# Kernel optimization log

Measured on AMD Instinct MI355X. Metric: run time of the kernel, lower is better.

Reference implementation:

```python
import jax, jax.numpy as jnp
import numpy as np

B, SQ, SK, D = 8, 2048, 768, 768  # SK must equal D for layer_combine concat to typecheck


def setup_inputs() -> dict:
    key = jax.random.key(0)
    ks = jax.random.split(key, 13)
    s = 0.02
    return {
        "query": jax.random.normal(ks[0], (B, SQ, D), jnp.float32),
        "key_matrix": jax.random.normal(ks[1], (B, SK, D), jnp.float32),
        "value_matrix": jax.random.normal(ks[2], (B, SK, D), jnp.float32),
        "prev_layer": jax.random.normal(ks[3], (SK, D), jnp.float32) * s,
        "attention_mask": jax.random.randint(ks[4], (B, 1, SK), 0, 2, jnp.int32),
        "Wq": jax.random.normal(ks[5], (D, D), jnp.float32) * s,
        "bq": jax.random.normal(ks[6], (D,), jnp.float32) * s,
        "Wk": jax.random.normal(ks[7], (D, D), jnp.float32) * s,
        "bk": jax.random.normal(ks[8], (D,), jnp.float32) * s,
        "Wv": jax.random.normal(ks[9], (D, D), jnp.float32) * s,
        "bv": jax.random.normal(ks[10], (D,), jnp.float32) * s,
        "Wc": jax.random.normal(ks[11], (D, 2 * D), jnp.float32) * s,
        "bc": jax.random.normal(ks[12], (D,), jnp.float32) * s,
    }


def reference(query, key_matrix, value_matrix, prev_layer, attention_mask,
              Wq, bq, Wk, bk, Wv, bv, Wc, bc):
    # Linear projections (torch Linear: x @ W.T + b)
    Q = query @ Wq.T + bq                      # [B, SQ, D]
    K = key_matrix @ Wk.T + bk                 # [B, SK, D]
    V = value_matrix @ Wv.T + bv               # computed but unused when prev_layer given (faithful)
    scale = 1.0 / np.sqrt(D).astype(np.float32)
    scores = jnp.einsum('bqd,bkd->bqk', Q, K) * scale  # [B, SQ, SK]
    scores = jnp.where(attention_mask == 0, jnp.float32(-1e9), scores)
    # prev-layer integration: matmul + concat + linear combine
    layer_attn = scores @ prev_layer           # [B, SQ, D]
    combined = jnp.concatenate([scores, layer_attn], axis=-1)  # [B, SQ, 2D]
    out = combined @ Wc.T + bc                 # [B, SQ, D]
    return out
```

## Files before the change

### kernel.cpp

```cpp
#include <hip/hip_runtime.h>
#include <hip/hip_bf16.h>


typedef __attribute__((ext_vector_type(8))) short short8;
typedef __attribute__((ext_vector_type(4))) float f32x4;

#define SCALE 0.03608439182435161f

__device__ inline unsigned short f2bf(float x) {
  unsigned int u = __builtin_bit_cast(unsigned int, x);
  u = (u + 0x7fffu + ((u >> 16) & 1u)) >> 16;
  return (unsigned short)u;
}
__device__ inline float bf2f(unsigned short h) {
  return __builtin_bit_cast(float, ((unsigned int)h) << 16);
}

__global__ void k_cvt8(const float* __restrict__ s, unsigned short* __restrict__ d, int n8) {
  int i = blockIdx.x * 256 + threadIdx.x;
  if (i >= n8) return;
  const float4* s4 = reinterpret_cast<const float4*>(s);
  float4 v0 = s4[2 * i], v1 = s4[2 * i + 1];
  ushort4* d4 = reinterpret_cast<ushort4*>(d);
  d4[2 * i]     = make_ushort4(f2bf(v0.x), f2bf(v0.y), f2bf(v0.z), f2bf(v0.w));
  d4[2 * i + 1] = make_ushort4(f2bf(v1.x), f2bf(v1.y), f2bf(v1.z), f2bf(v1.w));
}

__global__ void k_prep(const float* __restrict__ prev, const float* __restrict__ Wc,
                       unsigned short* __restrict__ prev_bf,
                       unsigned short* __restrict__ Wc2_bf) {
  int g = blockIdx.x;
  int region = g / 576;
  int idx = (g - region * 576) * 256 + threadIdx.x;
  float4 v;
  unsigned short* dst;
  if (region == 0) { v = reinterpret_cast<const float4*>(prev)[idx]; dst = prev_bf; }
  else {
    int r = idx / 192, c4 = (idx - r * 192) * 4;
    v = *reinterpret_cast<const float4*>(Wc + (long long)r * 1536 + 768 + c4);
    dst = Wc2_bf;
  }
  reinterpret_cast<ushort4*>(dst)[idx] = make_ushort4(f2bf(v.x), f2bf(v.y), f2bf(v.z), f2bf(v.w));
}

__global__ void k_tcvt(const float* __restrict__ Wq, const float* __restrict__ Wk,
                       const float* __restrict__ key, const int* __restrict__ mask,
                       unsigned short* __restrict__ WqT, unsigned short* __restrict__ WkT,
                       unsigned short* __restrict__ keyzT) {
  __shared__ float t[64][65];
  int z = blockIdx.z;
  const float* src;
  unsigned short* dst;
  const int* mb = nullptr;
  if (z == 0) { src = Wq; dst = WqT; }
  else if (z == 1) { src = Wk; dst = WkT; }
  else {
    int b = z - 2;
    src = key + (long long)b * 589824;
    dst = keyzT + (long long)b * 589824;
    mb = mask + b * 768;
  }
  int bx = blockIdx.x * 64, by = blockIdx.y * 64;
  int tx = threadIdx.x & 63, ty = threadIdx.x >> 6;
  #pragma unroll
  for (int i = 0; i < 64; i += 4) {
    float v = src[(long long)(by + ty + i) * 768 + bx + tx];
    if (mb) v = mb[by + ty + i] ? v : 0.0f;
    t[ty + i][tx] = v;
  }
  __syncthreads();
  #pragma unroll
  for (int i = 0; i < 64; i += 4)
    dst[(long long)(bx + ty + i) * 768 + by + tx] = f2bf(t[tx][ty + i]);
}

__global__ void k_sums(const unsigned short* __restrict__ WqT,
                       const unsigned short* __restrict__ WkT,
                       const float* __restrict__ bk, const float* __restrict__ bq,
                       const float* __restrict__ Mt, const int* __restrict__ mask,
                       float* __restrict__ u, float* __restrict__ w3,
                       float* __restrict__ s1, float* __restrict__ sm0) {
  int gw = blockIdx.x * 4 + (threadIdx.x >> 6);
  int lane = threadIdx.x & 63;
  if (gw < 1536) {
    const unsigned short* wrow = (gw < 768) ? (WqT + (long long)gw * 768)
                                            : (WkT + (long long)(gw - 768) * 768);
    const float* vec = (gw < 768) ? bk : bq;
    float s = 0.f;
    for (int j = lane; j < 768; j += 64) s += bf2f(wrow[j]) * vec[j];
    #pragma unroll
    for (int off = 32; off > 0; off >>= 1) s += __shfl_down(s, off, 64);
    if (lane == 0) { if (gw < 768) u[gw] = s; else w3[gw - 768] = s; }
  } else {
    int g2 = gw - 1536;
    int b = g2 / 768, d2 = g2 - b * 768;
    if (b >= 8) return;
    const int* mb = mask + b * 768;
    const float* mrow = Mt + (long long)d2 * 768;
    float a1 = 0.f, a0 = 0.f;
    for (int k = lane; k < 768; k += 64) {
      float v = mrow[k];
      if (mb[k]) a1 += v; else a0 += v;
    }
    #pragma unroll
    for (int off = 32; off > 0; off >>= 1) {
      a1 += __shfl_down(a1, off, 64);
      a0 += __shfl_down(a0, off, 64);
    }
    if (lane == 0) { s1[g2] = a1; sm0[g2] = a0; }
  }
}

__global__ void k_row(const unsigned short* __restrict__ Tt, const float* __restrict__ w3,
                      const float* __restrict__ s1, const float* __restrict__ sm0,
                      const float* __restrict__ bq, const float* __restrict__ bk,
                      const float* __restrict__ bc, float* __restrict__ row) {
  int gw = blockIdx.x * 4 + (threadIdx.x >> 6);
  int lane = threadIdx.x & 63;
  int b = gw / 768, d2 = gw - b * 768;
  if (b >= 8) return;
  const unsigned short* trow = Tt + ((long long)b * 768 + d2) * 768;
  float st = 0.f, sbb = 0.f;
  for (int j = lane; j < 768; j += 64) {
    st += bf2f(trow[j]) * w3[j];
    sbb += bq[j] * bk[j];
  }
  #pragma unroll
  for (int off = 32; off > 0; off >>= 1) {
    st += __shfl_down(st, off, 64);
    sbb += __shfl_down(sbb, off, 64);
  }
  if (lane == 0)
    row[gw] = bc[d2] - 1e9f * sm0[gw] + SCALE * (st + sbb * s1[gw]);
}

template <int MODE>
__global__ __launch_bounds__(256) void gemm_nt(
    const unsigned short* __restrict__ A, long long aStr, int lda,
    const unsigned short* __restrict__ B, long long bStr, int ldb,
    float* __restrict__ Cf, unsigned short* __restrict__ Cbf,
    long long cStr, int ldc,
    const float* __restrict__ aux, const float* __restrict__ aux2)
{
  constexpr int BM = 64, BN = 64, BK = 64;
  __shared__ __align__(16) char As[BM * BK * 2];
  __shared__ __align__(16) char Bs[BN * BK * 2];

  const int gx = gridDim.x, gy = gridDim.y;
  const int nwg = gx * gy * (int)gridDim.z;
  int lin = blockIdx.x + gx * (blockIdx.y + gy * blockIdx.z);
  int qq = nwg >> 3, rr = nwg & 7, xcd = lin & 7, loc = lin >> 3;
  int swz = (xcd < rr ? xcd * (qq + 1) : rr * (qq + 1) + (xcd - rr) * qq) + loc;
  int bz = swz / (gx * gy);
  int rem = swz - bz * gx * gy;
  int by = rem / gx, bx = rem - by * gx;

  const int b = bz;
  const unsigned short* Ab = A + (long long)b * aStr;
  const unsigned short* Bb = B + (long long)b * bStr;
  const int m0 = by * BM, n0 = bx * BN;

  const int tid = threadIdx.x;
  const int w = tid >> 6, lane = tid & 63;
  const int wr = w >> 1, wc = w & 1;
  const int fr = lane & 15, fq = lane >> 4;

  f32x4 acc[2][2] = {};

  for (int kt = 0; kt < 768; kt += BK) {
    __syncthreads();
    #pragma unroll
    for (int t = 0; t < 2; ++t) {
      int g = t * 256 + tid;
      int row = g >> 3, s = g & 7;
      int sg = (s - row) & 7;
      const unsigned short* ga = Ab + (long long)(m0 + row) * lda + kt + sg * 8;
      __builtin_amdgcn_global_load_lds(
          (const __attribute__((address_space(1))) void*)ga,
          (__attribute__((address_space(3))) void*)(As + g * 16), 16, 0, 0);
    }
    #pragma unroll
    for (int t = 0; t < 2; ++t) {
      int g = t * 256 + tid;
      int row = g >> 3, s = g & 7;
      int sg = (s - row) & 7;
      const unsigned short* gb = Bb + (long long)(n0 + row) * ldb + kt + sg * 8;
      __builtin_amdgcn_global_load_lds(
          (const __attribute__((address_space(1))) void*)gb,
          (__attribute__((address_space(3))) void*)(Bs + g * 16), 16, 0, 0);
    }
    __syncthreads();

    #pragma unroll
    for (int kk = 0; kk < 2; ++kk) {
      short8 af[2], bfr[2];
      #pragma unroll
      for (int i = 0; i < 2; ++i) {
        int r = wr * 32 + i * 16 + fr;
        int sgi = ((kk * 4 + fq) + r) & 7;
        af[i] = *reinterpret_cast<const short8*>(As + r * 128 + sgi * 16);
      }
      #pragma unroll
      for (int j = 0; j < 2; ++j) {
        int r = wc * 32 + j * 16 + fr;
        int sgj = ((kk * 4 + fq) + r) & 7;
        bfr[j] = *reinterpret_cast<const short8*>(Bs + r * 128 + sgj * 16);
      }
      #pragma unroll
      for (int i = 0; i < 2; ++i)
        #pragma unroll
        for (int j = 0; j < 2; ++j)
          acc[i][j] = __builtin_amdgcn_mfma_f32_16x16x32_bf16(af[i], bfr[j], acc[i][j], 0, 0, 0);
    }
  }

  #pragma unroll
  for (int i = 0; i < 2; ++i)
    #pragma unroll
    for (int j = 0; j < 2; ++j)
      #pragma unroll
      for (int r = 0; r < 4; ++r) {
        int row = m0 + wr * 32 + i * 16 + fq * 4 + r;
        int col = n0 + wc * 32 + j * 16 + fr;
        float v = acc[i][j][r];
        if constexpr (MODE == 0) {
          v += aux[(long long)row * 1536 + col];
          Cf[(long long)row * 768 + col] = v;
          Cbf[(long long)row * 768 + col] = f2bf(v);
        } else if constexpr (MODE == 2) {
          Cbf[(long long)b * cStr + (long long)row * ldc + col] = f2bf(v);
        } else {
          v += aux[b * 768 + row] * aux2[col];
          Cbf[(long long)b * cStr + (long long)row * ldc + col] = f2bf(v);
        }
      }
}

__global__ __launch_bounds__(512, 1) void g5_pipe(
    const unsigned short* __restrict__ A,
    const unsigned short* __restrict__ B,
    float* __restrict__ C, const float* __restrict__ rowv)
{
  __shared__ __align__(16) char As[3][256 * 128];
  __shared__ __align__(16) char Bs[2][192 * 128];

  int lin = blockIdx.x + 4 * (blockIdx.y + 8 * blockIdx.z);
  int swz = (lin & 7) * 32 + (lin >> 3);
  int bz = swz >> 5;
  int rem = swz & 31;
  int by = rem >> 2, bx = rem & 3;

  const int b = bz;
  const int m0 = by * 256, n0 = bx * 192;
  const unsigned short* Ab = A + (long long)b * 1572864;
  const unsigned short* Bb = B + (long long)b * 589824;

  const int tid = threadIdx.x;
  const int w = tid >> 6, lane = tid & 63;
  const int wr = w >> 2, wn = w & 3;
  const int fr = lane & 15, fq = lane >> 4;

  f32x4 acc[8][3] = {};

  auto stageA = [&](int buf, int kt, int s0, int ns) {
    for (int s = s0; s < s0 + ns; ++s) {
      int g = s * 512 + tid;
      int row = g >> 3, slot = g & 7;
      int sg = (slot - row) & 7;
      const unsigned short* ga = Ab + (long long)(m0 + row) * 768 + kt + sg * 8;
      __builtin_amdgcn_global_load_lds(
          (const __attribute__((address_space(1))) void*)ga,
          (__attribute__((address_space(3))) void*)(&As[buf][0] + g * 16), 16, 0, 0);
    }
  };
  auto stageB = [&](int buf, int kt, int s0, int ns) {
    for (int s = s0; s < s0 + ns; ++s) {
      int g = s * 512 + tid;
      int row = g >> 3, slot = g & 7;
      int sg = (slot - row) & 7;
      const unsigned short* gb = Bb + (long long)(n0 + row) * 768 + kt + sg * 8;
      __builtin_amdgcn_global_load_lds(
          (const __attribute__((address_space(1))) void*)gb,
          (__attribute__((address_space(3))) void*)(&Bs[buf][0] + g * 16), 16, 0, 0);
    }
  };

  stageA(0, 0, 0, 4);
  stageB(0, 0, 0, 3);
  stageA(1, 64, 0, 4);
  asm volatile("s_waitcnt vmcnt(4)" ::: "memory");
  __builtin_amdgcn_s_barrier();

  for (int t = 0; t < 12; ++t) {
    const char* as = &As[t % 3][0];
    const char* bs = &Bs[t & 1][0];
    const int ktn1 = (t + 1) * 64, ktn2 = (t + 2) * 64;
    short8 a0[4], a1[4], bb[3];

    #pragma unroll
    for (int i = 0; i < 4; ++i) {
      int r = wr * 128 + i * 16 + fr;
      a0[i] = *reinterpret_cast<const short8*>(as + r * 128 + (((fq) + r) & 7) * 16);
    }
    #pragma unroll
    for (int j = 0; j < 3; ++j) {
      int r = wn * 48 + j * 16 + fr;
      bb[j] = *reinterpret_cast<const short8*>(bs + r * 128 + (((fq) + r) & 7) * 16);
    }
    if (t < 11) stageB((t + 1) & 1, ktn1, 0, 2);
    __builtin_amdgcn_s_barrier();
    __builtin_amdgcn_s_setprio(1);
    #pragma unroll
    for (int i = 0; i < 4; ++i)
      #pragma unroll
      for (int j = 0; j < 3; ++j)
        acc[i][j] = __builtin_amdgcn_mfma_f32_16x16x32_bf16(a0[i], bb[j], acc[i][j], 0, 0, 0);
    __builtin_amdgcn_s_setprio(0);
    __builtin_amdgcn_s_barrier();

    #pragma unroll
    for (int i = 0; i < 4; ++i) {
      int r = wr * 128 + (4 + i) * 16 + fr;
      a1[i] = *reinterpret_cast<const short8*>(as + r * 128 + (((fq) + r) & 7) * 16);
    }
    if (t < 11) stageB((t + 1) & 1, ktn1, 2, 1);
    if (t < 10) stageA((t + 2) % 3, ktn2, 0, 2);
    __builtin_amdgcn_s_barrier();
    __builtin_amdgcn_s_setprio(1);
    #pragma unroll
    for (int i = 0; i < 4; ++i)
      #pragma unroll
      for (int j = 0; j < 3; ++j)
        acc[4 + i][j] = __builtin_amdgcn_mfma_f32_16x16x32_bf16(a1[i], bb[j], acc[4 + i][j], 0, 0, 0);
    __builtin_amdgcn_s_setprio(0);
    __builtin_amdgcn_s_barrier();

    #pragma unroll
    for (int i = 0; i < 4; ++i) {
      int r = wr * 128 + i * 16 + fr;
      a0[i] = *reinterpret_cast<const short8*>(as + r * 128 + (((4 + fq) + r) & 7) * 16);
    }
    #pragma unroll
    for (int j = 0; j < 3; ++j) {
      int r = wn * 48 + j * 16 + fr;
      bb[j] = *reinterpret_cast<const short8*>(bs + r * 128 + (((4 + fq) + r) & 7) * 16);
    }
    if (t < 10) stageA((t + 2) % 3, ktn2, 2, 2);
    __builtin_amdgcn_s_barrier();
    __builtin_amdgcn_s_setprio(1);
    #pragma unroll
    for (int i = 0; i < 4; ++i)
      #pragma unroll
      for (int j = 0; j < 3; ++j)
        acc[i][j] = __builtin_amdgcn_mfma_f32_16x16x32_bf16(a0[i], bb[j], acc[i][j], 0, 0, 0);
    __builtin_amdgcn_s_setprio(0);
    __builtin_amdgcn_s_barrier();

    #pragma unroll
    for (int i = 0; i < 4; ++i) {
      int r = wr * 128 + (4 + i) * 16 + fr;
      a1[i] = *reinterpret_cast<const short8*>(as + r * 128 + (((4 + fq) + r) & 7) * 16);
    }
    __builtin_amdgcn_s_barrier();
    __builtin_amdgcn_s_setprio(1);
    #pragma unroll
    for (int i = 0; i < 4; ++i)
      #pragma unroll
      for (int j = 0; j < 3; ++j)
        acc[4 + i][j] = __builtin_amdgcn_mfma_f32_16x16x32_bf16(a1[i], bb[j], acc[4 + i][j], 0, 0, 0);
    __builtin_amdgcn_s_setprio(0);

    if (t < 10)       asm volatile("s_waitcnt vmcnt(4)" ::: "memory");
    else if (t == 10) asm volatile("s_waitcnt vmcnt(0)" ::: "memory");
    __builtin_amdgcn_s_barrier();
  }

  const long long ob = (long long)b * 1572864;
  #pragma unroll
  for (int i = 0; i < 8; ++i)
    #pragma unroll
    for (int j = 0; j < 3; ++j)
      #pragma unroll
      for (int r = 0; r < 4; ++r) {
        int row = m0 + wr * 128 + i * 16 + fq * 4 + r;
        int col = n0 + wn * 48 + j * 16 + fr;
        C[ob + (long long)row * 768 + col] = acc[i][j][r] * SCALE + rowv[b * 768 + col];
      }
}

extern "C" void kernel_launch(void* const* d_in, const int* in_sizes, int n_in,
                              void* d_out, int out_size, void* d_ws, size_t ws_size,
                              hipStream_t stream)
{
  const float* query = (const float*)d_in[0];
  const float* key   = (const float*)d_in[1];
  const float* prev  = (const float*)d_in[3];
  const int*   mask  = (const int*)d_in[4];
  const float* Wq    = (const float*)d_in[5];
  const float* bq    = (const float*)d_in[6];
  const float* Wk    = (const float*)d_in[7];
  const float* bk    = (const float*)d_in[8];
  const float* Wc    = (const float*)d_in[11];
  const float* bc    = (const float*)d_in[12];
  float* out = (float*)d_out;

  char* p = (char*)d_ws;
  size_t off = 0;
  auto alloc = [&](size_t bytes) {
    char* r = p + off;
    off += (bytes + 255) & ~(size_t)255;
    return r;
  };
  unsigned short* query_bf = (unsigned short*)alloc(12582912ull * 2);
  unsigned short* keyzT_bf = (unsigned short*)alloc(4718592ull * 2);
  unsigned short* WqT_bf   = (unsigned short*)alloc(589824ull * 2);
  unsigned short* WkT_bf   = (unsigned short*)alloc(589824ull * 2);
  unsigned short* prev_bf  = (unsigned short*)alloc(589824ull * 2);
  unsigned short* Wc2_bf   = (unsigned short*)alloc(589824ull * 2);
  float*          Mt_f     = (float*)alloc(589824ull * 4);
  unsigned short* Mt_bf    = (unsigned short*)alloc(589824ull * 2);
  unsigned short* W2_bf    = (unsigned short*)alloc(589824ull * 2);
  unsigned short* Tt_bf    = (unsigned short*)alloc(4718592ull * 2);
  unsigned short* Pt_bf    = (unsigned short*)alloc(4718592ull * 2);
  float*          s1f      = (float*)alloc(6144ull * 4);
  float*          sm0f     = (float*)alloc(6144ull * 4);
  float*          uv       = (float*)alloc(768ull * 4);
  float*          w3v      = (float*)alloc(768ull * 4);
  float*          rowv     = (float*)alloc(6144ull * 4);
  (void)ws_size; (void)in_sizes; (void)n_in; (void)out_size;

  k_cvt8<<<dim3(6144), dim3(256), 0, stream>>>(query, query_bf, 1572864);
  k_tcvt<<<dim3(12, 12, 10), dim3(256), 0, stream>>>(Wq, Wk, key, mask,
                                                     WqT_bf, WkT_bf, keyzT_bf);
  k_prep<<<dim3(1152), dim3(256), 0, stream>>>(prev, Wc, prev_bf, Wc2_bf);

  gemm_nt<0><<<dim3(12, 12, 1), dim3(256), 0, stream>>>(
      Wc2_bf, 0ll, 768, prev_bf, 0ll, 768, Mt_f, Mt_bf, 0ll, 768,
      Wc, (const float*)nullptr);
  gemm_nt<2><<<dim3(12, 12, 1), dim3(256), 0, stream>>>(
      WqT_bf, 0ll, 768, WkT_bf, 0ll, 768, (float*)nullptr, W2_bf, 0ll, 768,
      (const float*)nullptr, (const float*)nullptr);
  k_sums<<<dim3(1920), dim3(256), 0, stream>>>(WqT_bf, WkT_bf, bk, bq, Mt_f, mask,
                                               uv, w3v, s1f, sm0f);
  gemm_nt<2><<<dim3(12, 12, 8), dim3(256), 0, stream>>>(
      Mt_bf, 0ll, 768, keyzT_bf, 589824ll, 768, (float*)nullptr, Tt_bf,
      589824ll, 768, (const float*)nullptr, (const float*)nullptr);
  gemm_nt<5><<<dim3(12, 12, 8), dim3(256), 0, stream>>>(
      Tt_bf, 589824ll, 768, W2_bf, 0ll, 768, (float*)nullptr, Pt_bf,
      589824ll, 768, s1f, uv);
  k_row<<<dim3(1536), dim3(256), 0, stream>>>(Tt_bf, w3v, s1f, sm0f, bq, bk, bc, rowv);
  g5_pipe<<<dim3(4, 8, 8), dim3(512), 0, stream>>>(query_bf, Pt_bf, out, rowv);
}
```

Measured before the change: 115.4 us.

## Merge two weight GEMMs into one launch and simplify g5 pipeline schedule

Two independent 768x768 weight GEMMs (Wc2·prev and WqT·WkT) now run as one launch with a z-dimension of 2, saving a kernel launch and letting both fill the GPU together. The main g5_pipe loop drops its hand-interleaved four-phase schedule, which used split stage loads and many intra-iteration barriers. It now issues all prefetches for the next tiles at the top of each iteration and then runs two k-substeps, each loading all 8 A fragments and 3 B fragments before its MFMAs. This removes barrier overhead but loses fine-grained interleaving of loads with compute and raises register pressure with 8 A fragments live.

```diff
diff --git a/kernel.cpp b/kernel.cpp
--- a/kernel.cpp
+++ b/kernel.cpp
@@ -134,40 +134,26 @@
     row[gw] = bc[d2] - 1e9f * sm0[gw] + SCALE * (st + sbb * s1[gw]);
 }
 
-template <int MODE>
-__global__ __launch_bounds__(256) void gemm_nt(
-    const unsigned short* __restrict__ A, long long aStr, int lda,
-    const unsigned short* __restrict__ B, long long bStr, int ldb,
-    float* __restrict__ Cf, unsigned short* __restrict__ Cbf,
-    long long cStr, int ldc,
-    const float* __restrict__ aux, const float* __restrict__ aux2)
-{
-  constexpr int BM = 64, BN = 64, BK = 64;
-  __shared__ __align__(16) char As[BM * BK * 2];
-  __shared__ __align__(16) char Bs[BN * BK * 2];
-
+__device__ inline void xcd_swz(int& bx, int& by, int& bz) {
   const int gx = gridDim.x, gy = gridDim.y;
   const int nwg = gx * gy * (int)gridDim.z;
   int lin = blockIdx.x + gx * (blockIdx.y + gy * blockIdx.z);
   int qq = nwg >> 3, rr = nwg & 7, xcd = lin & 7, loc = lin >> 3;
   int swz = (xcd < rr ? xcd * (qq + 1) : rr * (qq + 1) + (xcd - rr) * qq) + loc;
-  int bz = swz / (gx * gy);
+  bz = swz / (gx * gy);
   int rem = swz - bz * gx * gy;
-  int by = rem / gx, bx = rem - by * gx;
-
-  const int b = bz;
-  const unsigned short* Ab = A + (long long)b * aStr;
-  const unsigned short* Bb = B + (long long)b * bStr;
-  const int m0 = by * BM, n0 = bx * BN;
-
-  const int tid = threadIdx.x;
+  by = rem / gx;
+  bx = rem - by * gx;
+}
+
+__device__ inline void nt64_core(const unsigned short* Ab, int lda,
+                                 const unsigned short* Bb, int ldb,
+                                 int m0, int n0, int tid, f32x4 (&acc)[2][2],
+                                 char* As, char* Bs) {
   const int w = tid >> 6, lane = tid & 63;
   const int wr = w >> 1, wc = w & 1;
   const int fr = lane & 15, fq = lane >> 4;
-
-  f32x4 acc[2][2] = {};
-
-  for (int kt = 0; kt < 768; kt += BK) {
+  for (int kt = 0; kt < 768; kt += 64) {
     __syncthreads();
     #pragma unroll
     for (int t = 0; t < 2; ++t) {
@@ -190,21 +176,18 @@
           (__attribute__((address_space(3))) void*)(Bs + g * 16), 16, 0, 0);
     }
     __syncthreads();
-
     #pragma unroll
     for (int kk = 0; kk < 2; ++kk) {
       short8 af[2], bfr[2];
       #pragma unroll
       for (int i = 0; i < 2; ++i) {
         int r = wr * 32 + i * 16 + fr;
-        int sgi = ((kk * 4 + fq) + r) & 7;
-        af[i] = *reinterpret_cast<const short8*>(As + r * 128 + sgi * 16);
+        af[i] = *reinterpret_cast<const short8*>(As + r * 128 + (((kk * 4 + fq) + r) & 7) * 16);
       }
       #pragma unroll
       for (int j = 0; j < 2; ++j) {
         int r = wc * 32 + j * 16 + fr;
-        int sgj = ((kk * 4 + fq) + r) & 7;
-        bfr[j] = *reinterpret_cast<const short8*>(Bs + r * 128 + sgj * 16);
+        bfr[j] = *reinterpret_cast<const short8*>(Bs + r * 128 + (((kk * 4 + fq) + r) & 7) * 16);
       }
       #pragma unroll
       for (int i = 0; i < 2; ++i)
@@ -213,7 +196,28 @@
           acc[i][j] = __builtin_amdgcn_mfma_f32_16x16x32_bf16(af[i], bfr[j], acc[i][j], 0, 0, 0);
     }
   }
-
+}
+
+__global__ __launch_bounds__(256) void gemm_g1w2(
+    const unsigned short* __restrict__ Wc2_bf, const unsigned short* __restrict__ prev_bf,
+    const unsigned short* __restrict__ WqT_bf, const unsigned short* __restrict__ WkT_bf,
+    const float* __restrict__ Wc, float* __restrict__ Mt_f,
+    unsigned short* __restrict__ Mt_bf, unsigned short* __restrict__ W2_bf)
+{
+  __shared__ __align__(16) char As[64 * 128];
+  __shared__ __align__(16) char Bs[64 * 128];
+  int bx, by, bz;
+  xcd_swz(bx, by, bz);
+  const int m0 = by * 64, n0 = bx * 64;
+  const unsigned short* A = bz ? WqT_bf : Wc2_bf;
+  const unsigned short* B = bz ? WkT_bf : prev_bf;
+  const int tid = threadIdx.x;
+  f32x4 acc[2][2] = {};
+  nt64_core(A, 768, B, 768, m0, n0, tid, acc, As, Bs);
+
+  const int w = tid >> 6, lane = tid & 63;
+  const int wr = w >> 1, wc = w & 1;
+  const int fr = lane & 15, fq = lane >> 4;
   #pragma unroll
   for (int i = 0; i < 2; ++i)
     #pragma unroll
@@ -223,16 +227,48 @@
         int row = m0 + wr * 32 + i * 16 + fq * 4 + r;
         int col = n0 + wc * 32 + j * 16 + fr;
         float v = acc[i][j][r];
-        if constexpr (MODE == 0) {
-          v += aux[(long long)row * 1536 + col];
-          Cf[(long long)row * 768 + col] = v;
-          Cbf[(long long)row * 768 + col] = f2bf(v);
-        } else if constexpr (MODE == 2) {
-          Cbf[(long long)b * cStr + (long long)row * ldc + col] = f2bf(v);
+        if (bz == 0) {
+          v += Wc[(long long)row * 1536 + col];
+          Mt_f[(long long)row * 768 + col] = v;
+          Mt_bf[(long long)row * 768 + col] = f2bf(v);
         } else {
-          v += aux[b * 768 + row] * aux2[col];
-          Cbf[(long long)b * cStr + (long long)row * ldc + col] = f2bf(v);
+          W2_bf[(long long)row * 768 + col] = f2bf(v);
         }
+      }
+}
+
+template <int MODE>
+__global__ __launch_bounds__(256) void gemm_nt(
+    const unsigned short* __restrict__ A, long long aStr,
+    const unsigned short* __restrict__ B, long long bStr,
+    unsigned short* __restrict__ Cbf, long long cStr,
+    const float* __restrict__ aux, const float* __restrict__ aux2)
+{
+  __shared__ __align__(16) char As[64 * 128];
+  __shared__ __align__(16) char Bs[64 * 128];
+  int bx, by, bz;
+  xcd_swz(bx, by, bz);
+  const int b = bz;
+  const int m0 = by * 64, n0 = bx * 64;
+  const int tid = threadIdx.x;
+  f32x4 acc[2][2] = {};
+  nt64_core(A + (long long)b * aStr, 768, B + (long long)b * bStr, 768,
+            m0, n0, tid, acc, As, Bs);
+
+  const int w = tid >> 6, lane = tid & 63;
+  const int wr = w >> 1, wc = w & 1;
+  const int fr = lane & 15, fq = lane >> 4;
+  #pragma unroll
+  for (int i = 0; i < 2; ++i)
+    #pragma unroll
+    for (int j = 0; j < 2; ++j)
+      #pragma unroll
+      for (int r = 0; r < 4; ++r) {
+        int row = m0 + wr * 32 + i * 16 + fq * 4 + r;
+        int col = n0 + wc * 32 + j * 16 + fr;
+        float v = acc[i][j][r];
+        if constexpr (MODE == 5) v += aux[b * 768 + row] * aux2[col];
+        Cbf[(long long)b * cStr + (long long)row * 768 + col] = f2bf(v);
       }
 }
 
@@ -262,8 +298,9 @@
 
   f32x4 acc[8][3] = {};
 
-  auto stageA = [&](int buf, int kt, int s0, int ns) {
-    for (int s = s0; s < s0 + ns; ++s) {
+  auto stageA = [&](int buf, int kt) {
+    #pragma unroll
+    for (int s = 0; s < 4; ++s) {
       int g = s * 512 + tid;
       int row = g >> 3, slot = g & 7;
       int sg = (slot - row) & 7;
@@ -273,8 +310,9 @@
           (__attribute__((address_space(3))) void*)(&As[buf][0] + g * 16), 16, 0, 0);
     }
   };
-  auto stageB = [&](int buf, int kt, int s0, int ns) {
-    for (int s = s0; s < s0 + ns; ++s) {
+  auto stageB = [&](int buf, int kt) {
+    #pragma unroll
+    for (int s = 0; s < 3; ++s) {
       int g = s * 512 + tid;
       int row = g >> 3, slot = g & 7;
       int sg = (slot - row) & 7;
@@ -285,90 +323,40 @@
     }
   };
 
-  stageA(0, 0, 0, 4);
-  stageB(0, 0, 0, 3);
-  stageA(1, 64, 0, 4);
+  stageA(0, 0);
+  stageB(0, 0);
+  stageA(1, 64);
   asm volatile("s_waitcnt vmcnt(4)" ::: "memory");
   __builtin_amdgcn_s_barrier();
 
   for (int t = 0; t < 12; ++t) {
     const char* as = &As[t % 3][0];
     const char* bs = &Bs[t & 1][0];
-    const int ktn1 = (t + 1) * 64, ktn2 = (t + 2) * 64;
-    short8 a0[4], a1[4], bb[3];
-
-    #pragma unroll
-    for (int i = 0; i < 4; ++i) {
-      int r = wr * 128 + i * 16 + fr;
-      a0[i] = *reinterpret_cast<const short8*>(as + r * 128 + (((fq) + r) & 7) * 16);
-    }
-    #pragma unroll
-    for (int j = 0; j < 3; ++j) {
-      int r = wn * 48 + j * 16 + fr;
-      bb[j] = *reinterpret_cast<const short8*>(bs + r * 128 + (((fq) + r) & 7) * 16);
-    }
-    if (t < 11) stageB((t + 1) & 1, ktn1, 0, 2);
-    __builtin_amdgcn_s_barrier();
-    __builtin_amdgcn_s_setprio(1);
-    #pragma unroll
-    for (int i = 0; i < 4; ++i)
-      #pragma unroll
-      for (int j = 0; j < 3; ++j)
-        acc[i][j] = __builtin_amdgcn_mfma_f32_16x16x32_bf16(a0[i], bb[j], acc[i][j], 0, 0, 0);
-    __builtin_amdgcn_s_setprio(0);
-    __builtin_amdgcn_s_barrier();
-
-    #pragma unroll
-    for (int i = 0; i < 4; ++i) {
-      int r = wr * 128 + (4 + i) * 16 + fr;
-      a1[i] = *reinterpret_cast<const short8*>(as + r * 128 + (((fq) + r) & 7) * 16);
-    }
-    if (t < 11) stageB((t + 1) & 1, ktn1, 2, 1);
-    if (t < 10) stageA((t + 2) % 3, ktn2, 0, 2);
-    __builtin_amdgcn_s_barrier();
-    __builtin_amdgcn_s_setprio(1);
-    #pragma unroll
-    for (int i = 0; i < 4; ++i)
-      #pragma unroll
-      for (int j = 0; j < 3; ++j)
-        acc[4 + i][j] = __builtin_amdgcn_mfma_f32_16x16x32_bf16(a1[i], bb[j], acc[4 + i][j], 0, 0, 0);
-    __builtin_amdgcn_s_setprio(0);
-    __builtin_amdgcn_s_barrier();
-
-    #pragma unroll
-    for (int i = 0; i < 4; ++i) {
-      int r = wr * 128 + i * 16 + fr;
-      a0[i] = *reinterpret_cast<const short8*>(as + r * 128 + (((4 + fq) + r) & 7) * 16);
-    }
-    #pragma unroll
-    for (int j = 0; j < 3; ++j) {
-      int r = wn * 48 + j * 16 + fr;
-      bb[j] = *reinterpret_cast<const short8*>(bs + r * 128 + (((4 + fq) + r) & 7) * 16);
-    }
-    if (t < 10) stageA((t + 2) % 3, ktn2, 2, 2);
-    __builtin_amdgcn_s_barrier();
-    __builtin_amdgcn_s_setprio(1);
-    #pragma unroll
-    for (int i = 0; i < 4; ++i)
-      #pragma unroll
-      for (int j = 0; j < 3; ++j)
-        acc[i][j] = __builtin_amdgcn_mfma_f32_16x16x32_bf16(a0[i], bb[j], acc[i][j], 0, 0, 0);
-    __builtin_amdgcn_s_setprio(0);
-    __builtin_amdgcn_s_barrier();
-
-    #pragma unroll
-    for (int i = 0; i < 4; ++i) {
-      int r = wr * 128 + (4 + i) * 16 + fr;
-      a1[i] = *reinterpret_cast<const short8*>(as + r * 128 + (((4 + fq) + r) & 7) * 16);
-    }
-    __builtin_amdgcn_s_barrier();
-    __builtin_amdgcn_s_setprio(1);
-    #pragma unroll
-    for (int i = 0; i < 4; ++i)
-      #pragma unroll
-      for (int j = 0; j < 3; ++j)
-        acc[4 + i][j] = __builtin_amdgcn_mfma_f32_16x16x32_bf16(a1[i], bb[j], acc[4 + i][j], 0, 0, 0);
-    __builtin_amdgcn_s_setprio(0);
+
+    if (t < 11) stageB((t + 1) & 1, (t + 1) * 64);
+    if (t < 10) stageA((t + 2) % 3, (t + 2) * 64);
+
+    #pragma unroll
+    for (int kk = 0; kk < 2; ++kk) {
+      short8 a[8], bb[3];
+      #pragma unroll
+      for (int i = 0; i < 8; ++i) {
+        int r = wr * 128 + i * 16 + fr;
+        a[i] = *reinterpret_cast<const short8*>(as + r * 128 + (((kk * 4 + fq) + r) & 7) * 16);
+      }
+      #pragma unroll
+      for (int j = 0; j < 3; ++j) {
+        int r = wn * 48 + j * 16 + fr;
+        bb[j] = *reinterpret_cast<const short8*>(bs + r * 128 + (((kk * 4 + fq) + r) & 7) * 16);
+      }
+      __builtin_amdgcn_s_setprio(1);
+      #pragma unroll
+      for (int i = 0; i < 8; ++i)
+        #pragma unroll
+        for (int j = 0; j < 3; ++j)
+          acc[i][j] = __builtin_amdgcn_mfma_f32_16x16x32_bf16(a[i], bb[j], acc[i][j], 0, 0, 0);
+      __builtin_amdgcn_s_setprio(0);
+    }
 
     if (t < 10)       asm volatile("s_waitcnt vmcnt(4)" ::: "memory");
     else if (t == 10) asm volatile("s_waitcnt vmcnt(0)" ::: "memory");
@@ -434,20 +422,15 @@
                                                      WqT_bf, WkT_bf, keyzT_bf);
   k_prep<<<dim3(1152), dim3(256), 0, stream>>>(prev, Wc, prev_bf, Wc2_bf);
 
-  gemm_nt<0><<<dim3(12, 12, 1), dim3(256), 0, stream>>>(
-      Wc2_bf, 0ll, 768, prev_bf, 0ll, 768, Mt_f, Mt_bf, 0ll, 768,
-      Wc, (const float*)nullptr);
-  gemm_nt<2><<<dim3(12, 12, 1), dim3(256), 0, stream>>>(
-      WqT_bf, 0ll, 768, WkT_bf, 0ll, 768, (float*)nullptr, W2_bf, 0ll, 768,
-      (const float*)nullptr, (const float*)nullptr);
+  gemm_g1w2<<<dim3(12, 12, 2), dim3(256), 0, stream>>>(
+      Wc2_bf, prev_bf, WqT_bf, WkT_bf, Wc, Mt_f, Mt_bf, W2_bf);
   k_sums<<<dim3(1920), dim3(256), 0, stream>>>(WqT_bf, WkT_bf, bk, bq, Mt_f, mask,
                                                uv, w3v, s1f, sm0f);
   gemm_nt<2><<<dim3(12, 12, 8), dim3(256), 0, stream>>>(
-      Mt_bf, 0ll, 768, keyzT_bf, 589824ll, 768, (float*)nullptr, Tt_bf,
-      589824ll, 768, (const float*)nullptr, (const float*)nullptr);
+      Mt_bf, 0ll, keyzT_bf, 589824ll, Tt_bf, 589824ll,
+      (const float*)nullptr, (const float*)nullptr);
   gemm_nt<5><<<dim3(12, 12, 8), dim3(256), 0, stream>>>(
-      Tt_bf, 589824ll, 768, W2_bf, 0ll, 768, (float*)nullptr, Pt_bf,
-      589824ll, 768, s1f, uv);
+      Tt_bf, 589824ll, W2_bf, 0ll, Pt_bf, 589824ll, s1f, uv);
   k_row<<<dim3(1536), dim3(256), 0, stream>>>(Tt_bf, w3v, s1f, sm0f, bq, bk, bc, rowv);
   g5_pipe<<<dim3(4, 8, 8), dim3(512), 0, stream>>>(query_bf, Pt_bf, out, rowv);
 }
```

New measurement: 110.4 us. 4.4% less time.
